# Kernel optimization log

Hardware: AMD Instinct MI355X
Metric: run time of the kernel (lower is better)

The kernel has to match this reference:

```python
import jax, jax.numpy as jnp
import numpy as np

N_NODES = 100000
N_EDGES = 1000000
HIDDEN = 128
GROUPS = [[0, 1, 2], [3, 4, 5], [6, 7, 8]]  # model_ids[i]['volume_ids']
COMBOS = [(0, 0), (0, 1), (0, 2), (1, 1), (1, 2), (2, 2)]  # combinations with replacement
LN_EPS = 1e-5


def _ln(h, g, b):
    m = jnp.mean(h, axis=-1, keepdims=True)
    v = jnp.var(h, axis=-1, keepdims=True)
    return (h - m) * jax.lax.rsqrt(v + LN_EPS) * g + b


def setup_inputs() -> dict:
    key = jax.random.key(0)
    ks = jax.random.split(key, 8)
    C = len(COMBOS)
    s = 0.02
    x = jax.random.normal(ks[0], (N_NODES, HIDDEN), jnp.float32)
    e = jax.random.normal(ks[1], (N_EDGES, HIDDEN), jnp.float32)
    edge_index = jax.random.randint(ks[2], (2, N_EDGES), 0, N_NODES)
    volume_id = jax.random.randint(ks[3], (N_NODES,), 0, 9)
    W1 = (jax.random.normal(ks[4], (C, 3 * HIDDEN, HIDDEN), jnp.float32) * s)
    b1 = jnp.zeros((C, HIDDEN), jnp.float32)
    g1 = jnp.ones((C, HIDDEN), jnp.float32)
    be1 = jnp.zeros((C, HIDDEN), jnp.float32)
    W2 = (jax.random.normal(ks[5], (C, HIDDEN, HIDDEN), jnp.float32) * s)
    b2 = jnp.zeros((C, HIDDEN), jnp.float32)
    g2 = jnp.ones((C, HIDDEN), jnp.float32)
    be2 = jnp.zeros((C, HIDDEN), jnp.float32)
    W3 = (jax.random.normal(ks[6], (C, HIDDEN, 1), jnp.float32) * s)
    b3 = jnp.zeros((C, 1), jnp.float32)
    return dict(x=x, edge_index=edge_index, e=e, volume_id=volume_id,
                W1=W1, b1=b1, g1=g1, be1=be1,
                W2=W2, b2=b2, g2=g2, be2=be2,
                W3=W3, b3=b3)


def reference(x, edge_index, e, volume_id, W1, b1, g1, be1, W2, b2, g2, be2, W3, b3):
    # volume id -> group id lookup (constant, from hparams['model_ids'])
    group_of_vol = np.zeros(9, dtype=np.int32)
    for gi, vols in enumerate(GROUPS):
        group_of_vol[vols] = gi
    group_of_vol = jnp.asarray(group_of_vol)

    start, end = edge_index[0], edge_index[1]
    gs = group_of_vol[volume_id[start]]  # [E] group of start node
    ge = group_of_vol[volume_id[end]]    # [E] group of end node
    xs = x[start]                        # [E, H] gather
    xe = x[end]                          # [E, H] gather

    out = jnp.zeros((start.shape[0], 1), x.dtype)
    for c, (ga, gb) in enumerate(COMBOS):
        mask = (gs == ga) & (ge == gb)   # torch.isin on disjoint volume groups
        # split first Linear to avoid materializing concat([xs, xe, e])
        h = xs @ W1[c, :HIDDEN] + xe @ W1[c, HIDDEN:2 * HIDDEN] + e @ W1[c, 2 * HIDDEN:] + b1[c]
        h = jax.nn.relu(_ln(h, g1[c], be1[c]))
        h = jax.nn.relu(_ln(h @ W2[c] + b2[c], g2[c], be2[c]))
        logit = h @ W3[c] + b3[c]        # [E, 1]
        out = jnp.where(mask[:, None], logit, out)  # masked scatter into shared buffer
    return out
```

## Files before the change

kernel.cpp:

```cpp
#include <hip/hip_runtime.h>

#define E_EDGES 1000000
#define N_NODES 100000
#define HID 128

static constexpr int    WS_CMB  = 256;
static constexpr int    WS_LIST = 1000448;
static constexpr int    WS_W1F  = 5001984;
static constexpr int    WS_W2F  = 5591808;

typedef __bf16 bf16x8 __attribute__((ext_vector_type(8)));
typedef float  f32x4  __attribute__((ext_vector_type(4)));

__device__ __forceinline__ unsigned short f2bf(float f) {
    unsigned int u = __builtin_bit_cast(unsigned int, f);
    u = (u + 0x7FFFu + ((u >> 16) & 1u)) >> 16;
    return (unsigned short)u;
}

__global__ void k_wconv(const float* __restrict__ W1, const float* __restrict__ W2,
                        unsigned short* __restrict__ w1f, unsigned short* __restrict__ w2f) {
    int idx = blockIdx.x * 256 + threadIdx.x;
    if (idx < 294912) {
        int j = idx & 7, lane = (idx >> 3) & 63, nt = (idx >> 9) & 7;
        int t = idx >> 12;
        int c = t / 12, kt = t - c * 12;
        int k = kt * 32 + ((lane >> 4) << 3) + j;
        int n = (nt << 4) + (lane & 15);
        w1f[idx] = f2bf(W1[(c * 384 + k) * 128 + n]);
    } else {
        int i2 = idx - 294912;
        int j = i2 & 7, lane = (i2 >> 3) & 63, nt = (i2 >> 9) & 7;
        int t = i2 >> 12;
        int c = t >> 2, kt = t & 3;
        int k = kt * 32 + ((lane >> 4) << 3) + j;
        int n = (nt << 4) + (lane & 15);
        w2f[i2] = f2bf(W2[(c * 128 + k) * 128 + n]);
    }
}

__global__ void k_classify(const int* __restrict__ ei, const int* __restrict__ vol,
                           signed char* __restrict__ cmb, float* __restrict__ out,
                           int* __restrict__ counts) {
    __shared__ int bc[6];
    int tid = threadIdx.x;
    if (tid < 6) bc[tid] = 0;
    __syncthreads();
    int eid = blockIdx.x * 256 + tid;
    if (eid < E_EDGES) {
        int s = ei[eid], t = ei[E_EDGES + eid];
        int gs = vol[s] / 3, ge = vol[t] / 3;
        int cc = -1;
        if (gs <= ge) cc = (gs == 0 ? 0 : (gs == 1 ? 2 : 3)) + ge;
        cmb[eid] = (signed char)cc;
        if (cc < 0) out[eid] = 0.f;
        else atomicAdd(&bc[cc], 1);
    }
    __syncthreads();
    if (tid < 6 && bc[tid] > 0) atomicAdd(&counts[tid], bc[tid]);
}

__global__ void k_offsets(int* __restrict__ ws) {
    if (threadIdx.x == 0 && blockIdx.x == 0) {
        int* counts = ws;
        int* seg    = ws + 16;
        int* tile   = ws + 24;
        int acc = 0;
        for (int c = 0; c < 6; ++c) {
            seg[c]  = acc;
            tile[c] = acc >> 6;
            acc += ((counts[c] + 63) >> 6) << 6;
        }
        seg[6]  = acc;
        tile[6] = acc >> 6;
    }
}

__global__ void k_scatter(const signed char* __restrict__ cmb, int* __restrict__ list,
                          const int* __restrict__ seg, int* __restrict__ cursor) {
    __shared__ int bc[6], basep[6];
    int tid = threadIdx.x;
    if (tid < 6) bc[tid] = 0;
    __syncthreads();
    int eid = blockIdx.x * 256 + tid;
    int cc = -1, lp = 0;
    if (eid < E_EDGES) {
        cc = cmb[eid];
        if (cc >= 0) lp = atomicAdd(&bc[cc], 1);
    }
    __syncthreads();
    if (tid < 6) basep[tid] = bc[tid] > 0 ? atomicAdd(&cursor[tid], bc[tid]) : 0;
    __syncthreads();
    if (cc >= 0) list[seg[cc] + basep[cc] + lp] = eid;
}

__global__ __launch_bounds__(256) void k_mlp(
    const float* __restrict__ x, const int* __restrict__ ei, const float* __restrict__ efeat,
    const int* __restrict__ tile_tab, const int* __restrict__ list,
    const unsigned short* __restrict__ w1f, const unsigned short* __restrict__ w2f,
    const float* __restrict__ b1, const float* __restrict__ g1, const float* __restrict__ be1,
    const float* __restrict__ b2, const float* __restrict__ g2, const float* __restrict__ be2,
    const float* __restrict__ W3, const float* __restrict__ b3,
    float* __restrict__ out)
{
    __shared__ unsigned short Albuf[64 * 392];
    __shared__ int eids_s[64], sn[64], en[64];

    int b = blockIdx.x;
    if (b >= tile_tab[6]) return;
    int c = 0;
#pragma unroll
    for (int k = 1; k < 6; ++k) if (b >= tile_tab[k]) c = k;
    int tb = b - tile_tab[c];
    int segbase = tile_tab[c] * 64;
    int tid = threadIdx.x;

    if (tid < 64) {
        int eid = list[segbase + tb * 64 + tid];
        eids_s[tid] = eid;
        int a = 0, bb = 0;
        if (eid >= 0) { a = ei[eid]; bb = ei[E_EDGES + eid]; }
        sn[tid] = a; en[tid] = bb;
    }
    __syncthreads();

#pragma unroll
    for (int sec = 0; sec < 3; ++sec) {
#pragma unroll
        for (int it = 0; it < 8; ++it) {
            int i = tid + it * 256;
            int r = i >> 5, c4 = i & 31;
            float4 v = make_float4(0.f, 0.f, 0.f, 0.f);
            if (eids_s[r] >= 0) {
                const float* src;
                if (sec == 0)      src = x + (long)sn[r] * 128;
                else if (sec == 1) src = x + (long)en[r] * 128;
                else               src = efeat + (long)eids_s[r] * 128;
                v = ((const float4*)src)[c4];
            }
            ushort4 u;
            u.x = f2bf(v.x); u.y = f2bf(v.y); u.z = f2bf(v.z); u.w = f2bf(v.w);
            *(ushort4*)(&Albuf[r * 392 + sec * 128 + c4 * 4]) = u;
        }
    }
    __syncthreads();

    int lane = tid & 63;
    int wv = tid >> 6;
    int colb = lane & 15;
    int quad = lane >> 4;

    const bf16x8* w1v = (const bf16x8*)w1f;
    const bf16x8* w2v = (const bf16x8*)w2f;
    const f32x4 zero4 = {0.f, 0.f, 0.f, 0.f};

    f32x4 acc[8];
#pragma unroll
    for (int nt = 0; nt < 8; ++nt) acc[nt] = zero4;
    int arow = (wv * 16 + colb) * 392 + quad * 8;
#pragma unroll
    for (int kt = 0; kt < 12; ++kt) {
        bf16x8 af = *(const bf16x8*)(&Albuf[arow + kt * 32]);
        int wbase = ((c * 12 + kt) * 8) * 64 + lane;
#pragma unroll
        for (int nt = 0; nt < 8; ++nt) {
            bf16x8 bf = w1v[wbase + nt * 64];
            acc[nt] = __builtin_amdgcn_mfma_f32_16x16x32_bf16(af, bf, acc[nt], 0, 0, 0);
        }
    }

    float pb[8], pg[8], pe[8];
#pragma unroll
    for (int nt = 0; nt < 8; ++nt) {
        int col = c * 128 + colb + nt * 16;
        pb[nt] = b1[col]; pg[nt] = g1[col]; pe[nt] = be1[col];
    }
    float sum[4] = {0, 0, 0, 0}, sq[4] = {0, 0, 0, 0};
#pragma unroll
    for (int nt = 0; nt < 8; ++nt)
#pragma unroll
        for (int r = 0; r < 4; ++r) {
            float v = acc[nt][r] + pb[nt];
            acc[nt][r] = v;
            sum[r] += v; sq[r] += v * v;
        }
#pragma unroll
    for (int m = 1; m < 16; m <<= 1)
#pragma unroll
        for (int r = 0; r < 4; ++r) {
            sum[r] += __shfl_xor(sum[r], m);
            sq[r]  += __shfl_xor(sq[r], m);
        }
    float mean_[4], rstd_[4];
#pragma unroll
    for (int r = 0; r < 4; ++r) {
        float mu = sum[r] * 0.0078125f;
        float var = sq[r] * 0.0078125f - mu * mu;
        mean_[r] = mu;
        rstd_[r] = rsqrtf(var + 1e-5f);
    }
    int h1base = wv * 6272;
#pragma unroll
    for (int nt = 0; nt < 8; ++nt)
#pragma unroll
        for (int r = 0; r < 4; ++r) {
            float v = (acc[nt][r] - mean_[r]) * rstd_[r] * pg[nt] + pe[nt];
            v = fmaxf(v, 0.f);
            Albuf[h1base + (quad * 4 + r) * 136 + colb + nt * 16] = f2bf(v);
        }

    f32x4 acc2[8];
#pragma unroll
    for (int nt = 0; nt < 8; ++nt) acc2[nt] = zero4;
    int h1row = wv * 6272 + colb * 136 + quad * 8;
#pragma unroll
    for (int kt = 0; kt < 4; ++kt) {
        bf16x8 af = *(const bf16x8*)(&Albuf[h1row + kt * 32]);
        int wbase = ((c * 4 + kt) * 8) * 64 + lane;
#pragma unroll
        for (int nt = 0; nt < 8; ++nt) {
            bf16x8 bf = w2v[wbase + nt * 64];
            acc2[nt] = __builtin_amdgcn_mfma_f32_16x16x32_bf16(af, bf, acc2[nt], 0, 0, 0);
        }
    }

#pragma unroll
    for (int nt = 0; nt < 8; ++nt) {
        int col = c * 128 + colb + nt * 16;
        pb[nt] = b2[col]; pg[nt] = g2[col]; pe[nt] = be2[col];
    }
#pragma unroll
    for (int r = 0; r < 4; ++r) { sum[r] = 0.f; sq[r] = 0.f; }
#pragma unroll
    for (int nt = 0; nt < 8; ++nt)
#pragma unroll
        for (int r = 0; r < 4; ++r) {
            float v = acc2[nt][r] + pb[nt];
            acc2[nt][r] = v;
            sum[r] += v; sq[r] += v * v;
        }
#pragma unroll
    for (int m = 1; m < 16; m <<= 1)
#pragma unroll
        for (int r = 0; r < 4; ++r) {
            sum[r] += __shfl_xor(sum[r], m);
            sq[r]  += __shfl_xor(sq[r], m);
        }
#pragma unroll
    for (int r = 0; r < 4; ++r) {
        float mu = sum[r] * 0.0078125f;
        float var = sq[r] * 0.0078125f - mu * mu;
        mean_[r] = mu;
        rstd_[r] = rsqrtf(var + 1e-5f);
    }
    float w3v[8];
#pragma unroll
    for (int nt = 0; nt < 8; ++nt) w3v[nt] = W3[c * 128 + colb + nt * 16];
    float part[4] = {0, 0, 0, 0};
#pragma unroll
    for (int nt = 0; nt < 8; ++nt)
#pragma unroll
        for (int r = 0; r < 4; ++r) {
            float v = (acc2[nt][r] - mean_[r]) * rstd_[r] * pg[nt] + pe[nt];
            v = fmaxf(v, 0.f);
            part[r] += v * w3v[nt];
        }
#pragma unroll
    for (int m = 1; m < 16; m <<= 1)
#pragma unroll
        for (int r = 0; r < 4; ++r) part[r] += __shfl_xor(part[r], m);

    float b3v = b3[c];
    if (colb == 0) {
#pragma unroll
        for (int r = 0; r < 4; ++r) {
            int eid = eids_s[wv * 16 + quad * 4 + r];
            if (eid >= 0) out[eid] = part[r] + b3v;
        }
    }
}

extern "C" void kernel_launch(void* const* d_in, const int* in_sizes, int n_in,
                              void* d_out, int out_size, void* d_ws, size_t ws_size,
                              hipStream_t stream) {
    const float* x    = (const float*)d_in[0];
    const int*   ei   = (const int*)d_in[1];
    const float* e    = (const float*)d_in[2];
    const int*   vol  = (const int*)d_in[3];
    const float* W1   = (const float*)d_in[4];
    const float* b1   = (const float*)d_in[5];
    const float* g1   = (const float*)d_in[6];
    const float* be1  = (const float*)d_in[7];
    const float* W2   = (const float*)d_in[8];
    const float* b2   = (const float*)d_in[9];
    const float* g2   = (const float*)d_in[10];
    const float* be2  = (const float*)d_in[11];
    const float* W3   = (const float*)d_in[12];
    const float* b3   = (const float*)d_in[13];
    float* out = (float*)d_out;
    char* wsb = (char*)d_ws;

    hipMemsetAsync(wsb, 0, 256, stream);
    hipMemsetAsync(wsb + WS_LIST, 0xFF, (E_EDGES + 384) * sizeof(int), stream);

    k_wconv<<<1536, 256, 0, stream>>>(W1, W2,
        (unsigned short*)(wsb + WS_W1F), (unsigned short*)(wsb + WS_W2F));
    k_classify<<<(E_EDGES + 255) / 256, 256, 0, stream>>>(ei, vol,
        (signed char*)(wsb + WS_CMB), out, (int*)wsb);
    k_offsets<<<1, 64, 0, stream>>>((int*)wsb);
    k_scatter<<<(E_EDGES + 255) / 256, 256, 0, stream>>>(
        (const signed char*)(wsb + WS_CMB), (int*)(wsb + WS_LIST),
        (const int*)(wsb + 64), (int*)(wsb + 32));
    k_mlp<<<E_EDGES / 64 + 6, 256, 0, stream>>>(
        x, ei, e, (const int*)(wsb + 96), (const int*)(wsb + WS_LIST),
        (const unsigned short*)(wsb + WS_W1F), (const unsigned short*)(wsb + WS_W2F),
        b1, g1, be1, b2, g2, be2, W3, b3, out);
}
```

Measured before the change: 1.078 ms.

## Make each wave own a 32-edge tile and load A operands straight from global

The MLP kernel is restructured so each wavefront handles its own 32-edge tile, made of two 16-row MFMA groups that share every W1/W2 fragment load. The gathered node and edge features are read from global memory directly into registers with software prefetch, instead of being staged through a 64-row LDS buffer behind block-wide barriers. LDS then holds only the hidden activations per wave, and launch bounds request 4 blocks per CU to raise occupancy. Segment padding drops from 64 to 32 edges. In exchange, register pressure rises from the doubled accumulators, and each lane now makes strided 32-byte global reads.

```diff
diff --git a/kernel.cpp b/kernel.cpp
--- a/kernel.cpp
+++ b/kernel.cpp
@@ -68,11 +68,11 @@
         int acc = 0;
         for (int c = 0; c < 6; ++c) {
             seg[c]  = acc;
-            tile[c] = acc >> 6;
-            acc += ((counts[c] + 63) >> 6) << 6;
+            tile[c] = acc >> 5;
+            acc += ((counts[c] + 31) >> 5) << 5;
         }
         seg[6]  = acc;
-        tile[6] = acc >> 6;
+        tile[6] = acc >> 5;
     }
 }
 
@@ -94,7 +94,99 @@
     if (cc >= 0) list[seg[cc] + basep[cc] + lp] = eid;
 }
 
-__global__ __launch_bounds__(256) void k_mlp(
+__device__ __forceinline__ void ln1_store(f32x4* acc, const float* __restrict__ b1,
+    const float* __restrict__ g1, const float* __restrict__ be1,
+    int cb, int colb, int quad, unsigned short* hrow) {
+    float sum[4] = {0,0,0,0}, sq[4] = {0,0,0,0};
+#pragma unroll
+    for (int nt = 0; nt < 8; ++nt) {
+        float bb = b1[cb + colb + nt * 16];
+#pragma unroll
+        for (int r = 0; r < 4; ++r) {
+            float v = acc[nt][r] + bb;
+            acc[nt][r] = v; sum[r] += v; sq[r] += v * v;
+        }
+    }
+#pragma unroll
+    for (int m = 1; m < 16; m <<= 1)
+#pragma unroll
+        for (int r = 0; r < 4; ++r) {
+            sum[r] += __shfl_xor(sum[r], m);
+            sq[r]  += __shfl_xor(sq[r], m);
+        }
+    float mu[4], rs[4];
+#pragma unroll
+    for (int r = 0; r < 4; ++r) {
+        mu[r] = sum[r] * 0.0078125f;
+        float var = sq[r] * 0.0078125f - mu[r] * mu[r];
+        rs[r] = rsqrtf(var + 1e-5f);
+    }
+#pragma unroll
+    for (int nt = 0; nt < 8; ++nt) {
+        float gg = g1[cb + colb + nt * 16], ee = be1[cb + colb + nt * 16];
+#pragma unroll
+        for (int r = 0; r < 4; ++r) {
+            float v = (acc[nt][r] - mu[r]) * rs[r] * gg + ee;
+            v = fmaxf(v, 0.f);
+            hrow[(quad * 4 + r) * 136 + colb + nt * 16] =
+                __builtin_bit_cast(unsigned short, (__bf16)v);
+        }
+    }
+}
+
+__device__ __forceinline__ float ln2_dot(f32x4* acc, const float* __restrict__ b2,
+    const float* __restrict__ g2, const float* __restrict__ be2,
+    const float* __restrict__ W3, int cb, int colb, int quad) {
+    float sum[4] = {0,0,0,0}, sq[4] = {0,0,0,0};
+#pragma unroll
+    for (int nt = 0; nt < 8; ++nt) {
+        float bb = b2[cb + colb + nt * 16];
+#pragma unroll
+        for (int r = 0; r < 4; ++r) {
+            float v = acc[nt][r] + bb;
+            acc[nt][r] = v; sum[r] += v; sq[r] += v * v;
+        }
+    }
+#pragma unroll
+    for (int m = 1; m < 16; m <<= 1)
+#pragma unroll
+        for (int r = 0; r < 4; ++r) {
+            sum[r] += __shfl_xor(sum[r], m);
+            sq[r]  += __shfl_xor(sq[r], m);
+        }
+    float mu[4], rs[4];
+#pragma unroll
+    for (int r = 0; r < 4; ++r) {
+        mu[r] = sum[r] * 0.0078125f;
+        float var = sq[r] * 0.0078125f - mu[r] * mu[r];
+        rs[r] = rsqrtf(var + 1e-5f);
+    }
+    float part[4] = {0,0,0,0};
+#pragma unroll
+    for (int nt = 0; nt < 8; ++nt) {
+        float gg = g2[cb + colb + nt * 16], ee = be2[cb + colb + nt * 16];
+        float w3 = W3[cb + colb + nt * 16];
+#pragma unroll
+        for (int r = 0; r < 4; ++r) {
+            float v = (acc[nt][r] - mu[r]) * rs[r] * gg + ee;
+            v = fmaxf(v, 0.f);
+            part[r] += v * w3;
+        }
+    }
+#pragma unroll
+    for (int m = 1; m < 16; m <<= 1)
+#pragma unroll
+        for (int r = 0; r < 4; ++r) part[r] += __shfl_xor(part[r], m);
+    float vout = 0.f;
+#pragma unroll
+    for (int r = 0; r < 4; ++r) {
+        float t = __shfl(part[r], (colb >> 2) << 4);
+        if ((colb & 3) == r) vout = t;
+    }
+    return vout;
+}
+
+__global__ __launch_bounds__(256, 4) void k_mlp(
     const float* __restrict__ x, const int* __restrict__ ei, const float* __restrict__ efeat,
     const int* __restrict__ tile_tab, const int* __restrict__ list,
     const unsigned short* __restrict__ w1f, const unsigned short* __restrict__ w2f,
@@ -103,180 +195,97 @@
     const float* __restrict__ W3, const float* __restrict__ b3,
     float* __restrict__ out)
 {
-    __shared__ unsigned short Albuf[64 * 392];
-    __shared__ int eids_s[64], sn[64], en[64];
-
-    int b = blockIdx.x;
-    if (b >= tile_tab[6]) return;
+    __shared__ unsigned short H1[4 * 4352];
+
+    int tid  = threadIdx.x;
+    int wv   = tid >> 6, lane = tid & 63;
+    int colb = lane & 15, quad = lane >> 4;
+
+    int t32 = blockIdx.x * 4 + wv;
+    if (t32 >= tile_tab[6]) return;
     int c = 0;
 #pragma unroll
-    for (int k = 1; k < 6; ++k) if (b >= tile_tab[k]) c = k;
-    int tb = b - tile_tab[c];
-    int segbase = tile_tab[c] * 64;
-    int tid = threadIdx.x;
-
-    if (tid < 64) {
-        int eid = list[segbase + tb * 64 + tid];
-        eids_s[tid] = eid;
-        int a = 0, bb = 0;
-        if (eid >= 0) { a = ei[eid]; bb = ei[E_EDGES + eid]; }
-        sn[tid] = a; en[tid] = bb;
-    }
-    __syncthreads();
-
-#pragma unroll
-    for (int sec = 0; sec < 3; ++sec) {
-#pragma unroll
-        for (int it = 0; it < 8; ++it) {
-            int i = tid + it * 256;
-            int r = i >> 5, c4 = i & 31;
-            float4 v = make_float4(0.f, 0.f, 0.f, 0.f);
-            if (eids_s[r] >= 0) {
-                const float* src;
-                if (sec == 0)      src = x + (long)sn[r] * 128;
-                else if (sec == 1) src = x + (long)en[r] * 128;
-                else               src = efeat + (long)eids_s[r] * 128;
-                v = ((const float4*)src)[c4];
-            }
-            ushort4 u;
-            u.x = f2bf(v.x); u.y = f2bf(v.y); u.z = f2bf(v.z); u.w = f2bf(v.w);
-            *(ushort4*)(&Albuf[r * 392 + sec * 128 + c4 * 4]) = u;
-        }
-    }
-    __syncthreads();
-
-    int lane = tid & 63;
-    int wv = tid >> 6;
-    int colb = lane & 15;
-    int quad = lane >> 4;
+    for (int k = 1; k < 6; ++k) c += (t32 >= tile_tab[k]);
+
+    int lb = t32 * 32;
+    int f  = list[lb];
+    int e0 = list[lb + colb];
+    int e1 = list[lb + 16 + colb];
+    int a0 = e0 >= 0 ? e0 : f;
+    int a1 = e1 >= 0 ? e1 : f;
+
+    int s0 = ei[a0], t0 = ei[E_EDGES + a0];
+    int s1 = ei[a1], t1 = ei[E_EDGES + a1];
+    const float* base0[3] = { x + (size_t)s0 * 128, x + (size_t)t0 * 128, efeat + (size_t)a0 * 128 };
+    const float* base1[3] = { x + (size_t)s1 * 128, x + (size_t)t1 * 128, efeat + (size_t)a1 * 128 };
 
     const bf16x8* w1v = (const bf16x8*)w1f;
     const bf16x8* w2v = (const bf16x8*)w2f;
     const f32x4 zero4 = {0.f, 0.f, 0.f, 0.f};
-
-    f32x4 acc[8];
-#pragma unroll
-    for (int nt = 0; nt < 8; ++nt) acc[nt] = zero4;
-    int arow = (wv * 16 + colb) * 392 + quad * 8;
+    int cb = c * 128;
+
+    f32x4 acc0[8], acc1[8];
+#pragma unroll
+    for (int nt = 0; nt < 8; ++nt) { acc0[nt] = zero4; acc1[nt] = zero4; }
+
+    float4 p00, p01, p10, p11;
+    {
+        const float4* q0 = (const float4*)(base0[0] + quad * 8);
+        p00 = q0[0]; p01 = q0[1];
+        const float4* q1 = (const float4*)(base1[0] + quad * 8);
+        p10 = q1[0]; p11 = q1[1];
+    }
 #pragma unroll
     for (int kt = 0; kt < 12; ++kt) {
-        bf16x8 af = *(const bf16x8*)(&Albuf[arow + kt * 32]);
-        int wbase = ((c * 12 + kt) * 8) * 64 + lane;
+        float4 n00, n01, n10, n11;
+        if (kt < 11) {
+            int k1 = kt + 1, sec = k1 >> 2, ko = k1 & 3;
+            const float4* q0 = (const float4*)(base0[sec] + ko * 32 + quad * 8);
+            n00 = q0[0]; n01 = q0[1];
+            const float4* q1 = (const float4*)(base1[sec] + ko * 32 + quad * 8);
+            n10 = q1[0]; n11 = q1[1];
+        }
+        bf16x8 af0, af1;
+        af0[0] = (__bf16)p00.x; af0[1] = (__bf16)p00.y; af0[2] = (__bf16)p00.z; af0[3] = (__bf16)p00.w;
+        af0[4] = (__bf16)p01.x; af0[5] = (__bf16)p01.y; af0[6] = (__bf16)p01.z; af0[7] = (__bf16)p01.w;
+        af1[0] = (__bf16)p10.x; af1[1] = (__bf16)p10.y; af1[2] = (__bf16)p10.z; af1[3] = (__bf16)p10.w;
+        af1[4] = (__bf16)p11.x; af1[5] = (__bf16)p11.y; af1[6] = (__bf16)p11.z; af1[7] = (__bf16)p11.w;
+        int wbase = c * 6144 + kt * 512 + lane;
 #pragma unroll
         for (int nt = 0; nt < 8; ++nt) {
             bf16x8 bf = w1v[wbase + nt * 64];
-            acc[nt] = __builtin_amdgcn_mfma_f32_16x16x32_bf16(af, bf, acc[nt], 0, 0, 0);
-        }
-    }
-
-    float pb[8], pg[8], pe[8];
-#pragma unroll
-    for (int nt = 0; nt < 8; ++nt) {
-        int col = c * 128 + colb + nt * 16;
-        pb[nt] = b1[col]; pg[nt] = g1[col]; pe[nt] = be1[col];
-    }
-    float sum[4] = {0, 0, 0, 0}, sq[4] = {0, 0, 0, 0};
-#pragma unroll
-    for (int nt = 0; nt < 8; ++nt)
-#pragma unroll
-        for (int r = 0; r < 4; ++r) {
-            float v = acc[nt][r] + pb[nt];
-            acc[nt][r] = v;
-            sum[r] += v; sq[r] += v * v;
-        }
-#pragma unroll
-    for (int m = 1; m < 16; m <<= 1)
-#pragma unroll
-        for (int r = 0; r < 4; ++r) {
-            sum[r] += __shfl_xor(sum[r], m);
-            sq[r]  += __shfl_xor(sq[r], m);
-        }
-    float mean_[4], rstd_[4];
-#pragma unroll
-    for (int r = 0; r < 4; ++r) {
-        float mu = sum[r] * 0.0078125f;
-        float var = sq[r] * 0.0078125f - mu * mu;
-        mean_[r] = mu;
-        rstd_[r] = rsqrtf(var + 1e-5f);
-    }
-    int h1base = wv * 6272;
-#pragma unroll
-    for (int nt = 0; nt < 8; ++nt)
-#pragma unroll
-        for (int r = 0; r < 4; ++r) {
-            float v = (acc[nt][r] - mean_[r]) * rstd_[r] * pg[nt] + pe[nt];
-            v = fmaxf(v, 0.f);
-            Albuf[h1base + (quad * 4 + r) * 136 + colb + nt * 16] = f2bf(v);
-        }
-
-    f32x4 acc2[8];
-#pragma unroll
-    for (int nt = 0; nt < 8; ++nt) acc2[nt] = zero4;
-    int h1row = wv * 6272 + colb * 136 + quad * 8;
+            acc0[nt] = __builtin_amdgcn_mfma_f32_16x16x32_bf16(af0, bf, acc0[nt], 0, 0, 0);
+            acc1[nt] = __builtin_amdgcn_mfma_f32_16x16x32_bf16(af1, bf, acc1[nt], 0, 0, 0);
+        }
+        p00 = n00; p01 = n01; p10 = n10; p11 = n11;
+    }
+
+    unsigned short* hg0 = &H1[wv * 4352];
+    unsigned short* hg1 = &H1[wv * 4352 + 16 * 136];
+    ln1_store(acc0, b1, g1, be1, cb, colb, quad, hg0);
+    ln1_store(acc1, b1, g1, be1, cb, colb, quad, hg1);
+
+#pragma unroll
+    for (int nt = 0; nt < 8; ++nt) { acc0[nt] = zero4; acc1[nt] = zero4; }
 #pragma unroll
     for (int kt = 0; kt < 4; ++kt) {
-        bf16x8 af = *(const bf16x8*)(&Albuf[h1row + kt * 32]);
-        int wbase = ((c * 4 + kt) * 8) * 64 + lane;
+        bf16x8 af0 = *(const bf16x8*)&hg0[colb * 136 + quad * 8 + kt * 32];
+        bf16x8 af1 = *(const bf16x8*)&hg1[colb * 136 + quad * 8 + kt * 32];
+        int wbase = c * 2048 + kt * 512 + lane;
 #pragma unroll
         for (int nt = 0; nt < 8; ++nt) {
             bf16x8 bf = w2v[wbase + nt * 64];
-            acc2[nt] = __builtin_amdgcn_mfma_f32_16x16x32_bf16(af, bf, acc2[nt], 0, 0, 0);
-        }
-    }
-
-#pragma unroll
-    for (int nt = 0; nt < 8; ++nt) {
-        int col = c * 128 + colb + nt * 16;
-        pb[nt] = b2[col]; pg[nt] = g2[col]; pe[nt] = be2[col];
-    }
-#pragma unroll
-    for (int r = 0; r < 4; ++r) { sum[r] = 0.f; sq[r] = 0.f; }
-#pragma unroll
-    for (int nt = 0; nt < 8; ++nt)
-#pragma unroll
-        for (int r = 0; r < 4; ++r) {
-            float v = acc2[nt][r] + pb[nt];
-            acc2[nt][r] = v;
-            sum[r] += v; sq[r] += v * v;
-        }
-#pragma unroll
-    for (int m = 1; m < 16; m <<= 1)
-#pragma unroll
-        for (int r = 0; r < 4; ++r) {
-            sum[r] += __shfl_xor(sum[r], m);
-            sq[r]  += __shfl_xor(sq[r], m);
-        }
-#pragma unroll
-    for (int r = 0; r < 4; ++r) {
-        float mu = sum[r] * 0.0078125f;
-        float var = sq[r] * 0.0078125f - mu * mu;
-        mean_[r] = mu;
-        rstd_[r] = rsqrtf(var + 1e-5f);
-    }
-    float w3v[8];
-#pragma unroll
-    for (int nt = 0; nt < 8; ++nt) w3v[nt] = W3[c * 128 + colb + nt * 16];
-    float part[4] = {0, 0, 0, 0};
-#pragma unroll
-    for (int nt = 0; nt < 8; ++nt)
-#pragma unroll
-        for (int r = 0; r < 4; ++r) {
-            float v = (acc2[nt][r] - mean_[r]) * rstd_[r] * pg[nt] + pe[nt];
-            v = fmaxf(v, 0.f);
-            part[r] += v * w3v[nt];
-        }
-#pragma unroll
-    for (int m = 1; m < 16; m <<= 1)
-#pragma unroll
-        for (int r = 0; r < 4; ++r) part[r] += __shfl_xor(part[r], m);
+            acc0[nt] = __builtin_amdgcn_mfma_f32_16x16x32_bf16(af0, bf, acc0[nt], 0, 0, 0);
+            acc1[nt] = __builtin_amdgcn_mfma_f32_16x16x32_bf16(af1, bf, acc1[nt], 0, 0, 0);
+        }
+    }
 
     float b3v = b3[c];
-    if (colb == 0) {
-#pragma unroll
-        for (int r = 0; r < 4; ++r) {
-            int eid = eids_s[wv * 16 + quad * 4 + r];
-            if (eid >= 0) out[eid] = part[r] + b3v;
-        }
+    float v0 = ln2_dot(acc0, b2, g2, be2, W3, cb, colb, quad);
+    float v1 = ln2_dot(acc1, b2, g2, be2, W3, cb, colb, quad);
+    if (quad == 0) {
+        if (e0 >= 0) out[e0] = v0 + b3v;
+        if (e1 >= 0) out[e1] = v1 + b3v;
     }
 }
 
@@ -311,7 +320,10 @@
     k_scatter<<<(E_EDGES + 255) / 256, 256, 0, stream>>>(
         (const signed char*)(wsb + WS_CMB), (int*)(wsb + WS_LIST),
         (const int*)(wsb + 64), (int*)(wsb + 32));
-    k_mlp<<<E_EDGES / 64 + 6, 256, 0, stream>>>(
+
+    int maxt32 = E_EDGES / 32 + 6;
+    int grid = (maxt32 + 3) / 4;
+    k_mlp<<<grid, 256, 0, stream>>>(
         x, ei, e, (const int*)(wsb + 96), (const int*)(wsb + WS_LIST),
         (const unsigned short*)(wsb + WS_W1F), (const unsigned short*)(wsb + WS_W2F),
         b1, g1, be1, b2, g2, be2, W3, b3, out);
```

Measured after the change: 1.127 ms. +4.6%, slower.
